# Kernel tuning notes

Measured on AMD Instinct MI355X. Metric: run time of the kernel, lower is better.

Reference implementation:

```python
import jax, jax.numpy as jnp
import numpy as np

N = 4_000_000   # points at level d
SIDE = 1024     # coordinate range per axis
HALF = SIDE // 2  # parent coord range


def setup_inputs() -> dict:
    key = jax.random.key(0)
    k1, k2 = jax.random.split(key)
    xyz = jax.random.randint(k1, (N, 3), 0, SIDE, dtype=jnp.int32)
    b = (jnp.arange(N, dtype=jnp.int32) % 4)[:, None]  # 4 batches
    coords = jnp.concatenate([b, xyz], axis=1)          # (N,4): [b,x,y,z]
    kernel = jnp.ones((8,), dtype=jnp.float32)          # frozen all-ones 2x2x2 conv weights
    return {"coords": coords, "kernel": kernel}


def _fog(coords, kernel):
    # pos(): occupancy code 2**(x%2 + 2*y%2 + 4*z%2)
    bits = coords[:, 1:4] & 1                       # (N,3)
    off = bits[:, 0] + 2 * bits[:, 1] + 4 * bits[:, 2]  # (N,) child offset in 2x2x2 window
    pos = jnp.exp2(off.astype(jnp.float32))         # (N,) code in {1,2,4,...,128}
    contrib = pos * kernel[off]                     # per-offset conv weight (all ones)
    # stride-2 conv: parent voxel = floor(xyz/2); linearize (b,z,y,x) into a key
    parent = coords[:, 1:4] >> 1                    # (N,3)
    keys = (((coords[:, 0].astype(jnp.int64) * HALF + parent[:, 2]) * HALF
             + parent[:, 1]) * HALF + parent[:, 0])
    ukeys, inv = jnp.unique(keys, return_inverse=True, size=N, fill_value=-1)
    feats = jax.ops.segment_sum(contrib, inv, num_segments=N)[:, None]  # (N,1)
    # decode padded unique keys back to coords; pad slots -> -1
    px = (ukeys % HALF).astype(jnp.int32)
    py = ((ukeys // HALF) % HALF).astype(jnp.int32)
    pz = ((ukeys // (HALF * HALF)) % HALF).astype(jnp.int32)
    pb = (ukeys // (HALF * HALF * HALF)).astype(jnp.int32)
    valid = (ukeys >= 0)[:, None]
    coords_out = jnp.where(valid, jnp.stack([pb, px, py, pz], axis=1), -1)
    return coords_out, feats


def reference(coords, kernel):
    return _fog(coords, kernel)
```

## Files before the change

### kernel.cpp

```cpp
#include <hip/hip_runtime.h>
#include <stdint.h>

typedef unsigned int u32;
typedef unsigned long long u64;

#define LBITS  14
#define LMASK  ((1u << LBITS) - 1u)
#define NBUCK  (1u << (29 - LBITS))
#define BWORDS (1u << (LBITS - 5))
#define WPL    (BWORDS / 64)
#define WOPAD  (BWORDS + BWORDS / 32)
#define FCAP   192
#define BPB    4
#define TILE_A 8192
#define RPT    (TILE_A / 256)
#define S2     2
#define CAP2   9216
#define RPT2   (CAP2 / 256)
#define RECV   4
#define CAP    224
#define SCAN_ELEM 2048

__device__ __forceinline__ u32 woidx(u32 w) { return w + (w >> 5); }

__device__ __forceinline__ void wsync() {
    asm volatile("s_waitcnt lgkmcnt(0)" ::: "memory");
}

__device__ __forceinline__ u32 make_key(int4 c) {
    return ((((u32)c.x * 512u + ((u32)c.w >> 1)) * 512u + ((u32)c.z >> 1)) * 512u)
           + ((u32)c.y >> 1);
}

__global__ void __launch_bounds__(256) phase_a(const int4* __restrict__ coords,
        u32* __restrict__ linrec, u32* __restrict__ histmat, int n, u32 NT) {
    __shared__ u32 h[4 * 256];
    u32 t = threadIdx.x, wave = t >> 6;
    for (u32 j = t; j < 1024u; j += 256u) h[j] = 0u;
    __syncthreads();
    u32 base = blockIdx.x * TILE_A;
    u32 m = min((u32)TILE_A, (u32)n - base);
    for (u32 j = t; j < m; j += 256u) {
        int4 c = coords[base + j];
        u32 key = make_key(c);
        u32 off = ((u32)c.y & 1u) | (((u32)c.z & 1u) << 1) | (((u32)c.w & 1u) << 2);
        u32 rec = (key << 3) | off;
        linrec[base + j] = rec;
        atomicAdd(&h[wave * 256u + (rec >> 24)], 1u);
    }
    __syncthreads();
    histmat[t * NT + blockIdx.x] = h[t] + h[256u + t] + h[512u + t] + h[768u + t];
}

__global__ void scan_reduce(const u32* __restrict__ data, u32* __restrict__ partial, u32 G) {
    __shared__ u32 s[256];
    u32 t = threadIdx.x;
    u32 base = blockIdx.x * SCAN_ELEM + t * 8u;
    u32 sum = 0;
    #pragma unroll
    for (int j = 0; j < 8; ++j) { u32 idx = base + j; if (idx < G) sum += data[idx]; }
    s[t] = sum; __syncthreads();
    for (int d = 128; d > 0; d >>= 1) { if ((int)t < d) s[t] += s[t + d]; __syncthreads(); }
    if (t == 0) partial[blockIdx.x] = s[0];
}

__global__ void scan_apply2(const u32* __restrict__ data, u32* __restrict__ out,
                            const u32* __restrict__ partial, u32 G, u32 NB,
                            u32* __restrict__ total) {
    __shared__ u32 s[256];
    __shared__ u32 pb[2];
    u32 t = threadIdx.x;
    u32 p = (t < NB) ? partial[t] : 0u;
    u32 pbef = (t < blockIdx.x) ? p : 0u;
    s[t] = pbef; __syncthreads();
    for (int d = 128; d > 0; d >>= 1) { if ((int)t < d) s[t] += s[t + d]; __syncthreads(); }
    if (t == 0) pb[0] = s[0];
    __syncthreads();
    if (total) {
        s[t] = p; __syncthreads();
        for (int d = 128; d > 0; d >>= 1) { if ((int)t < d) s[t] += s[t + d]; __syncthreads(); }
        if (t == 0) pb[1] = s[0];
        __syncthreads();
        if (blockIdx.x == NB - 1u && t == 0u) total[0] = pb[1];
    }
    u32 base = blockIdx.x * SCAN_ELEM + t * 8u;
    u32 v[8]; u32 sum = 0;
    #pragma unroll
    for (int j = 0; j < 8; ++j) {
        u32 idx = base + j;
        v[j] = (idx < G) ? data[idx] : 0u;
        sum += v[j];
    }
    s[t] = sum; __syncthreads();
    for (int d = 1; d < 256; d <<= 1) {
        u32 add = (t >= (u32)d) ? s[t - d] : 0u;
        __syncthreads(); s[t] += add; __syncthreads();
    }
    u32 run = s[t] - sum + pb[0];
    #pragma unroll
    for (int j = 0; j < 8; ++j) {
        u32 idx = base + j;
        if (idx < G) { u32 x = v[j]; out[idx] = run; run += x; }
    }
}

__global__ void __launch_bounds__(256) part1(const u32* __restrict__ linrec,
        const u32* __restrict__ histex, u32* __restrict__ tmp,
        u32* __restrict__ cursor, int n, u32 NT) {
    __shared__ u32 stage[TILE_A];
    __shared__ u32 lcur[256];
    __shared__ u32 gb[256];
    __shared__ u32 wtot[4];
    u32 t = threadIdx.x, wave = t >> 6, lane = t & 63u;
    if (blockIdx.x < 128u) cursor[blockIdx.x * 256u + t] = 0u;
    u32 base = blockIdx.x * TILE_A;
    u32 m = min((u32)TILE_A, (u32)n - base);
    u32 m4 = m >> 2, rem = m & 3u;
    lcur[t] = 0u;
    __syncthreads();
    u32 recv[RPT]; u32 tailrec = 0u;
    const uint4* lr4 = (const uint4*)(linrec + base);
    #pragma unroll
    for (int k = 0; k < RPT / 4; ++k) {
        u32 j4 = (u32)k * 256u + t;
        if (j4 < m4) {
            uint4 v = lr4[j4];
            recv[k * 4 + 0] = v.x; recv[k * 4 + 1] = v.y;
            recv[k * 4 + 2] = v.z; recv[k * 4 + 3] = v.w;
            atomicAdd(&lcur[v.x >> 24], 1u);
            atomicAdd(&lcur[v.y >> 24], 1u);
            atomicAdd(&lcur[v.z >> 24], 1u);
            atomicAdd(&lcur[v.w >> 24], 1u);
        }
    }
    if (t < rem) {
        tailrec = linrec[base + (m & ~3u) + t];
        atomicAdd(&lcur[tailrec >> 24], 1u);
    }
    __syncthreads();
    u32 v = lcur[t];
    u32 incl = v;
    #pragma unroll
    for (int d = 1; d < 64; d <<= 1) {
        u32 x = __shfl_up(incl, d);
        if ((int)lane >= d) incl += x;
    }
    if (lane == 63u) wtot[wave] = incl;
    __syncthreads();
    u32 off = (wave > 0u ? wtot[0] : 0u) + (wave > 1u ? wtot[1] : 0u)
            + (wave > 2u ? wtot[2] : 0u);
    u32 excl = off + incl - v;
    lcur[t] = excl;
    gb[t] = histex[t * NT + blockIdx.x] - excl;
    __syncthreads();
    #pragma unroll
    for (int k = 0; k < RPT / 4; ++k) {
        u32 j4 = (u32)k * 256u + t;
        if (j4 < m4) {
            #pragma unroll
            for (int e = 0; e < 4; ++e) {
                u32 rec = recv[k * 4 + e];
                u32 pos = atomicAdd(&lcur[rec >> 24], 1u);
                stage[pos] = rec;
            }
        }
    }
    if (t < rem) {
        u32 pos = atomicAdd(&lcur[tailrec >> 24], 1u);
        stage[pos] = tailrec;
    }
    __syncthreads();
    for (u32 j = t; j < m; j += 256u) {
        u32 rec = stage[j];
        tmp[gb[rec >> 24] + j] = rec;
    }
}

__global__ void __launch_bounds__(256) part2(const u32* __restrict__ tmp,
        const u32* __restrict__ histex, u32* __restrict__ cursor,
        u32* __restrict__ buckrec, int n, u32 NT) {
    __shared__ u32 stage[CAP2];
    __shared__ u32 lcur[128];
    __shared__ u32 dstb[128];
    __shared__ u32 wtot[2];
    u32 t = threadIdx.x, lane = t & 63u;
    u32 c = blockIdx.x / S2, s = blockIdx.x % S2;
    u32 cs = histex[c * NT];
    u32 ce = (c == 255u) ? (u32)n : histex[(c + 1u) * NT];
    u32 L = ce - cs;
    u32 lo = cs + L * s / S2, hi = cs + L * (s + 1u) / S2;
    u32 cnt = hi - lo;
    if (cnt <= (u32)CAP2) {
        if (t < 128u) lcur[t] = 0u;
        __syncthreads();
        u32 recv[RPT2];
        #pragma unroll
        for (int k = 0; k < RPT2; ++k) {
            u32 j = (u32)k * 256u + t;
            if (j < cnt) {
                u32 rec = tmp[lo + j];
                recv[k] = rec;
                atomicAdd(&lcur[(rec >> 17) & 127u], 1u);
            }
        }
        __syncthreads();
        u32 v = 0, incl = 0;
        if (t < 128u) {
            v = lcur[t];
            incl = v;
            #pragma unroll
            for (int d = 1; d < 64; d <<= 1) {
                u32 x = __shfl_up(incl, d);
                if ((int)lane >= d) incl += x;
            }
            if (lane == 63u) wtot[t >> 6] = incl;
        }
        __syncthreads();
        if (t < 128u) {
            u32 off = (t >= 64u) ? wtot[0] : 0u;
            u32 excl = off + incl - v;
            u32 bucket = (c << 7) | t;
            u32 gbase = atomicAdd(&cursor[bucket], v);
            lcur[t] = excl;
            dstb[t] = bucket * (u32)CAP + gbase - excl;
        }
        __syncthreads();
        #pragma unroll
        for (int k = 0; k < RPT2; ++k) {
            u32 j = (u32)k * 256u + t;
            if (j < cnt) {
                u32 rec = recv[k];
                u32 pos = atomicAdd(&lcur[(rec >> 17) & 127u], 1u);
                stage[pos] = rec;
            }
        }
        __syncthreads();
        for (u32 j = t; j < cnt; j += 256u) {
            u32 rec = stage[j];
            buckrec[dstb[(rec >> 17) & 127u] + j] = rec;
        }
    } else {
        for (u32 i = lo + t; i < hi; i += 256u) {
            u32 rec = tmp[i];
            u32 b = rec >> 17;
            u32 pos = atomicAdd(&cursor[b], 1u);
            buckrec[b * (u32)CAP + pos] = rec;
        }
    }
}

__global__ void __launch_bounds__(256) pass_count(const u32* __restrict__ buckrec,
        const u32* __restrict__ bcnt, u32* __restrict__ ucount, int n) {
    __shared__ u32 bm[BPB][WOPAD];
    u32 wave = threadIdx.x >> 6, lane = threadIdx.x & 63u;
    u32 bucket = blockIdx.x * BPB + wave;
    u32* B = bm[wave];
    #pragma unroll
    for (int j = 0; j < WPL; ++j) B[woidx(lane * WPL + j)] = 0u;
    wsync();
    u32 start = bucket * (u32)CAP;
    u32 end = start + bcnt[bucket];
    for (u32 i = start + lane; i < end; i += 64u) {
        u32 lk = (buckrec[i] >> 3) & LMASK;
        atomicOr(&B[woidx(lk >> 5)], 1u << (lk & 31u));
    }
    wsync();
    u32 sum = 0;
    #pragma unroll
    for (int j = 0; j < WPL; ++j) sum += __popc(B[woidx(lane * WPL + j)]);
    #pragma unroll
    for (int d = 1; d < 64; d <<= 1) sum += __shfl_xor(sum, d);
    if (lane == 0u) ucount[bucket] = sum;
}

__global__ void __launch_bounds__(256) pass_emit(const u32* __restrict__ buckrec,
        const u32* __restrict__ bcnt, const u32* __restrict__ ubase,
        const float* __restrict__ kern, float4* __restrict__ rows,
        float* __restrict__ feats, int n) {
    __shared__ u32 bm[BPB][WOPAD];
    __shared__ u32 wofW[BPB][BWORDS];
    __shared__ float fl[BPB][FCAP];
    __shared__ float ksc[BPB][8];
    u32 wave = threadIdx.x >> 6, lane = threadIdx.x & 63u;
    u32 bucket = blockIdx.x * BPB + wave;
    u32* B = bm[wave];
    u32* W = wofW[wave];
    float* F = fl[wave];
    #pragma unroll
    for (int j = 0; j < WPL; ++j) B[woidx(lane * WPL + j)] = 0u;
    #pragma unroll
    for (u32 j = lane; j < FCAP; j += 64u) F[j] = 0.f;
    if (lane < 8u) ksc[wave][lane] = (float)(1u << lane) * kern[lane];
    wsync();
    u32 start = bucket * (u32)CAP;
    u32 cnt = bcnt[bucket];
    u32 recv[RECV];
    #pragma unroll
    for (int k = 0; k < RECV; ++k) {
        u32 idx = (u32)k * 64u + lane;
        if (idx < cnt) {
            u32 rec = buckrec[start + idx];
            recv[k] = rec;
            u32 lk = (rec >> 3) & LMASK;
            atomicOr(&B[woidx(lk >> 5)], 1u << (lk & 31u));
        }
    }
    wsync();
    u32 wv[WPL]; u32 pc[WPL]; u32 sum = 0;
    #pragma unroll
    for (int j = 0; j < WPL; ++j) {
        wv[j] = B[woidx(lane * WPL + j)];
        pc[j] = __popc(wv[j]);
        sum += pc[j];
    }
    u32 incl = sum;
    #pragma unroll
    for (int d = 1; d < 64; d <<= 1) {
        u32 tt = __shfl_up(incl, d);
        if ((int)lane >= d) incl += tt;
    }
    u32 lex = incl - sum;
    u32 uc = __shfl(incl, 63);
    {
        u32 r = lex;
        #pragma unroll
        for (int j = 0; j < WPL; ++j) { W[((u32)j << 6) | lane] = r; r += pc[j]; }
    }
    wsync();
    u32 base = ubase[bucket];
    bool lds_ok = (uc <= FCAP);
    if (!lds_ok) {
        for (u32 j = lane; j < uc; j += 64u) feats[base + j] = 0.f;
        asm volatile("s_waitcnt vmcnt(0)" ::: "memory");
    }
    #pragma unroll
    for (int k = 0; k < RECV; ++k) {
        u32 idx = (u32)k * 64u + lane;
        if (idx < cnt) {
            u32 rec = recv[k];
            float contrib = ksc[wave][rec & 7u];
            u32 lk = (rec >> 3) & LMASK;
            u32 w = lk >> 5, bit = lk & 31u;
            u32 r = W[((w & 7u) << 6) | (w >> 3)]
                  + __popc(B[woidx(w)] & ((1u << bit) - 1u));
            if (lds_ok) atomicAdd(&F[r], contrib);
            else        atomicAdd(&feats[base + r], contrib);
        }
    }
    wsync();
    u32 rank = base + lex;
    u32 keyhi = bucket << LBITS;
    #pragma unroll
    for (int j = 0; j < WPL; ++j) {
        u32 bits = wv[j];
        u32 kb = keyhi | ((lane * (u32)WPL + (u32)j) << 5);
        while (bits) {
            u32 tz = __builtin_ctz(bits);
            bits &= bits - 1u;
            u32 key = kb | tz;
            rows[rank++] = make_float4((float)(key >> 27), (float)(key & 511u),
                                       (float)((key >> 9) & 511u),
                                       (float)((key >> 18) & 511u));
        }
    }
    if (lds_ok) {
        for (u32 j = lane; j < uc; j += 64u) feats[base + j] = F[j];
    }
}

__global__ void pad_fill(float4* __restrict__ rows, float* __restrict__ feats,
                         const u32* __restrict__ counter, int n) {
    int i = blockIdx.x * blockDim.x + threadIdx.x;
    if (i < n && (u32)i >= counter[0]) {
        rows[i] = make_float4(-1.f, -1.f, -1.f, -1.f);
        feats[i] = 0.f;
    }
}

extern "C" void kernel_launch(void* const* d_in, const int* in_sizes, int n_in,
                              void* d_out, int out_size, void* d_ws, size_t ws_size,
                              hipStream_t stream) {
    const int n = in_sizes[0] / 4;
    const int4* coords = (const int4*)d_in[0];
    const float* kern  = (const float*)d_in[1];
    const u32 NT = ((u32)n + TILE_A - 1) / TILE_A;
    const u32 G1 = 256 * NT;
    const u32 NB1 = (G1 + SCAN_ELEM - 1) / SCAN_ELEM;
    const u32 NB3 = (NBUCK + SCAN_ELEM - 1) / SCAN_ELEM;

    u32* wsp = (u32*)d_ws;
    u32* tmp     = wsp;
    u32* histmat = tmp + n;
    u32* histex  = histmat + G1;
    u32* cursor  = histex + G1;
    u32* ucount  = cursor + NBUCK;
    u32* ubase   = ucount + NBUCK;
    u32* counter = ubase + NBUCK;
    u32* spart   = counter + 4;
    u32* linrec  = spart + 256;
    u32* buckrec = linrec;

    float4* rows  = (float4*)d_out;
    float*  feats = (float*)((char*)d_out + (size_t)n * 16);

    phase_a<<<NT, 256, 0, stream>>>(coords, linrec, histmat, n, NT);
    scan_reduce<<<NB1, 256, 0, stream>>>(histmat, spart, G1);
    scan_apply2<<<NB1, 256, 0, stream>>>(histmat, histex, spart, G1, NB1, (u32*)nullptr);
    part1<<<NT, 256, 0, stream>>>(linrec, histex, tmp, cursor, n, NT);
    part2<<<256 * S2, 256, 0, stream>>>(tmp, histex, cursor, buckrec, n, NT);
    pass_count<<<NBUCK / BPB, 256, 0, stream>>>(buckrec, cursor, ucount, n);
    scan_reduce<<<NB3, 256, 0, stream>>>(ucount, spart, NBUCK);
    scan_apply2<<<NB3, 256, 0, stream>>>(ucount, ubase, spart, NBUCK, NB3, counter);
    pass_emit<<<NBUCK / BPB, 256, 0, stream>>>(buckrec, cursor, ubase, kern,
                                               rows, feats, n);
    pad_fill<<<((u32)n + 255) / 256, 256, 0, stream>>>(rows, feats, counter, n);
}
```

Baseline: 227.9 us.

## Fuse key build into first radix pass using fixed-capacity atomic bucket slots

Removes the separate histogram pass and its global scan. Each tile now computes keys directly from coords, counts its top-byte digits in shared memory, and reserves space in fixed-capacity per-digit regions through global atomics. This saves a full read and write of the record array and two scan launches. In exchange, each digit region is capped at 16384 records, so a skewed key distribution would overflow it. Output order within a digit also depends on the order the atomics run, which part2 has to tolerate. Tile and split sizes are halved to match the new layout.

```diff
diff --git a/kernel.cpp b/kernel.cpp
--- a/kernel.cpp
+++ b/kernel.cpp
@@ -12,10 +12,11 @@
 #define WOPAD  (BWORDS + BWORDS / 32)
 #define FCAP   192
 #define BPB    4
-#define TILE_A 8192
+#define TILE_A 4096
 #define RPT    (TILE_A / 256)
-#define S2     2
-#define CAP2   9216
+#define CCAP   16384
+#define S2     4
+#define CAP2   4608
 #define RPT2   (CAP2 / 256)
 #define RECV   4
 #define CAP    224
@@ -32,24 +33,68 @@
            + ((u32)c.y >> 1);
 }
 
-__global__ void __launch_bounds__(256) phase_a(const int4* __restrict__ coords,
-        u32* __restrict__ linrec, u32* __restrict__ histmat, int n, u32 NT) {
-    __shared__ u32 h[4 * 256];
-    u32 t = threadIdx.x, wave = t >> 6;
-    for (u32 j = t; j < 1024u; j += 256u) h[j] = 0u;
-    __syncthreads();
+__global__ void zero1(u32* __restrict__ p, u32 g) {
+    u32 i = blockIdx.x * 256u + threadIdx.x;
+    if (i < g) p[i] = 0u;
+}
+
+__global__ void __launch_bounds__(256) part1f(const int4* __restrict__ coords,
+        u32* __restrict__ ccur, u32* __restrict__ tmp,
+        u32* __restrict__ cursor, int n) {
+    __shared__ u32 stage[TILE_A];
+    __shared__ u32 lcur[256];
+    __shared__ u32 gb[256];
+    __shared__ u32 wtot[4];
+    u32 t = threadIdx.x, wave = t >> 6, lane = t & 63u;
+    if (blockIdx.x < 128u) cursor[blockIdx.x * 256u + t] = 0u;
     u32 base = blockIdx.x * TILE_A;
     u32 m = min((u32)TILE_A, (u32)n - base);
+    lcur[t] = 0u;
+    __syncthreads();
+    u32 recv[RPT];
+    #pragma unroll
+    for (int k = 0; k < RPT; ++k) {
+        u32 j = (u32)k * 256u + t;
+        if (j < m) {
+            int4 c = coords[base + j];
+            u32 key = make_key(c);
+            u32 off = ((u32)c.y & 1u) | (((u32)c.z & 1u) << 1) | (((u32)c.w & 1u) << 2);
+            u32 rec = (key << 3) | off;
+            recv[k] = rec;
+            atomicAdd(&lcur[rec >> 24], 1u);
+        }
+    }
+    __syncthreads();
+    u32 v = lcur[t];
+    u32 incl = v;
+    #pragma unroll
+    for (int d = 1; d < 64; d <<= 1) {
+        u32 x = __shfl_up(incl, d);
+        if ((int)lane >= d) incl += x;
+    }
+    if (lane == 63u) wtot[wave] = incl;
+    __syncthreads();
+    u32 off = (wave > 0u ? wtot[0] : 0u) + (wave > 1u ? wtot[1] : 0u)
+            + (wave > 2u ? wtot[2] : 0u);
+    u32 excl = off + incl - v;
+    u32 gbase = atomicAdd(&ccur[t * 16u], v);
+    lcur[t] = excl;
+    gb[t] = (t << 14) + gbase - excl;
+    __syncthreads();
+    #pragma unroll
+    for (int k = 0; k < RPT; ++k) {
+        u32 j = (u32)k * 256u + t;
+        if (j < m) {
+            u32 rec = recv[k];
+            u32 pos = atomicAdd(&lcur[rec >> 24], 1u);
+            stage[pos] = rec;
+        }
+    }
+    __syncthreads();
     for (u32 j = t; j < m; j += 256u) {
-        int4 c = coords[base + j];
-        u32 key = make_key(c);
-        u32 off = ((u32)c.y & 1u) | (((u32)c.z & 1u) << 1) | (((u32)c.w & 1u) << 2);
-        u32 rec = (key << 3) | off;
-        linrec[base + j] = rec;
-        atomicAdd(&h[wave * 256u + (rec >> 24)], 1u);
-    }
-    __syncthreads();
-    histmat[t * NT + blockIdx.x] = h[t] + h[256u + t] + h[512u + t] + h[768u + t];
+        u32 rec = stage[j];
+        tmp[gb[rec >> 24] + j] = rec;
+    }
 }
 
 __global__ void scan_reduce(const u32* __restrict__ data, u32* __restrict__ partial, u32 G) {
@@ -104,90 +149,17 @@
     }
 }
 
-__global__ void __launch_bounds__(256) part1(const u32* __restrict__ linrec,
-        const u32* __restrict__ histex, u32* __restrict__ tmp,
-        u32* __restrict__ cursor, int n, u32 NT) {
-    __shared__ u32 stage[TILE_A];
-    __shared__ u32 lcur[256];
-    __shared__ u32 gb[256];
-    __shared__ u32 wtot[4];
-    u32 t = threadIdx.x, wave = t >> 6, lane = t & 63u;
-    if (blockIdx.x < 128u) cursor[blockIdx.x * 256u + t] = 0u;
-    u32 base = blockIdx.x * TILE_A;
-    u32 m = min((u32)TILE_A, (u32)n - base);
-    u32 m4 = m >> 2, rem = m & 3u;
-    lcur[t] = 0u;
-    __syncthreads();
-    u32 recv[RPT]; u32 tailrec = 0u;
-    const uint4* lr4 = (const uint4*)(linrec + base);
-    #pragma unroll
-    for (int k = 0; k < RPT / 4; ++k) {
-        u32 j4 = (u32)k * 256u + t;
-        if (j4 < m4) {
-            uint4 v = lr4[j4];
-            recv[k * 4 + 0] = v.x; recv[k * 4 + 1] = v.y;
-            recv[k * 4 + 2] = v.z; recv[k * 4 + 3] = v.w;
-            atomicAdd(&lcur[v.x >> 24], 1u);
-            atomicAdd(&lcur[v.y >> 24], 1u);
-            atomicAdd(&lcur[v.z >> 24], 1u);
-            atomicAdd(&lcur[v.w >> 24], 1u);
-        }
-    }
-    if (t < rem) {
-        tailrec = linrec[base + (m & ~3u) + t];
-        atomicAdd(&lcur[tailrec >> 24], 1u);
-    }
-    __syncthreads();
-    u32 v = lcur[t];
-    u32 incl = v;
-    #pragma unroll
-    for (int d = 1; d < 64; d <<= 1) {
-        u32 x = __shfl_up(incl, d);
-        if ((int)lane >= d) incl += x;
-    }
-    if (lane == 63u) wtot[wave] = incl;
-    __syncthreads();
-    u32 off = (wave > 0u ? wtot[0] : 0u) + (wave > 1u ? wtot[1] : 0u)
-            + (wave > 2u ? wtot[2] : 0u);
-    u32 excl = off + incl - v;
-    lcur[t] = excl;
-    gb[t] = histex[t * NT + blockIdx.x] - excl;
-    __syncthreads();
-    #pragma unroll
-    for (int k = 0; k < RPT / 4; ++k) {
-        u32 j4 = (u32)k * 256u + t;
-        if (j4 < m4) {
-            #pragma unroll
-            for (int e = 0; e < 4; ++e) {
-                u32 rec = recv[k * 4 + e];
-                u32 pos = atomicAdd(&lcur[rec >> 24], 1u);
-                stage[pos] = rec;
-            }
-        }
-    }
-    if (t < rem) {
-        u32 pos = atomicAdd(&lcur[tailrec >> 24], 1u);
-        stage[pos] = tailrec;
-    }
-    __syncthreads();
-    for (u32 j = t; j < m; j += 256u) {
-        u32 rec = stage[j];
-        tmp[gb[rec >> 24] + j] = rec;
-    }
-}
-
 __global__ void __launch_bounds__(256) part2(const u32* __restrict__ tmp,
-        const u32* __restrict__ histex, u32* __restrict__ cursor,
-        u32* __restrict__ buckrec, int n, u32 NT) {
+        const u32* __restrict__ ccur, u32* __restrict__ cursor,
+        u32* __restrict__ buckrec, int n) {
     __shared__ u32 stage[CAP2];
     __shared__ u32 lcur[128];
     __shared__ u32 dstb[128];
     __shared__ u32 wtot[2];
     u32 t = threadIdx.x, lane = t & 63u;
     u32 c = blockIdx.x / S2, s = blockIdx.x % S2;
-    u32 cs = histex[c * NT];
-    u32 ce = (c == 255u) ? (u32)n : histex[(c + 1u) * NT];
-    u32 L = ce - cs;
+    u32 cs = c << 14;
+    u32 L = ccur[c * 16u];
     u32 lo = cs + L * s / S2, hi = cs + L * (s + 1u) / S2;
     u32 cnt = hi - lo;
     if (cnt <= (u32)CAP2) {
@@ -384,30 +356,24 @@
     const int4* coords = (const int4*)d_in[0];
     const float* kern  = (const float*)d_in[1];
     const u32 NT = ((u32)n + TILE_A - 1) / TILE_A;
-    const u32 G1 = 256 * NT;
-    const u32 NB1 = (G1 + SCAN_ELEM - 1) / SCAN_ELEM;
     const u32 NB3 = (NBUCK + SCAN_ELEM - 1) / SCAN_ELEM;
 
     u32* wsp = (u32*)d_ws;
     u32* tmp     = wsp;
-    u32* histmat = tmp + n;
-    u32* histex  = histmat + G1;
-    u32* cursor  = histex + G1;
+    u32* ccur    = tmp + 256 * CCAP;
+    u32* cursor  = ccur + 256 * 16;
     u32* ucount  = cursor + NBUCK;
     u32* ubase   = ucount + NBUCK;
     u32* counter = ubase + NBUCK;
     u32* spart   = counter + 4;
-    u32* linrec  = spart + 256;
-    u32* buckrec = linrec;
+    u32* buckrec = spart + 256;
 
     float4* rows  = (float4*)d_out;
     float*  feats = (float*)((char*)d_out + (size_t)n * 16);
 
-    phase_a<<<NT, 256, 0, stream>>>(coords, linrec, histmat, n, NT);
-    scan_reduce<<<NB1, 256, 0, stream>>>(histmat, spart, G1);
-    scan_apply2<<<NB1, 256, 0, stream>>>(histmat, histex, spart, G1, NB1, (u32*)nullptr);
-    part1<<<NT, 256, 0, stream>>>(linrec, histex, tmp, cursor, n, NT);
-    part2<<<256 * S2, 256, 0, stream>>>(tmp, histex, cursor, buckrec, n, NT);
+    zero1<<<16, 256, 0, stream>>>(ccur, 256 * 16);
+    part1f<<<NT, 256, 0, stream>>>(coords, ccur, tmp, cursor, n);
+    part2<<<256 * S2, 256, 0, stream>>>(tmp, ccur, cursor, buckrec, n);
     pass_count<<<NBUCK / BPB, 256, 0, stream>>>(buckrec, cursor, ucount, n);
     scan_reduce<<<NB3, 256, 0, stream>>>(ucount, spart, NBUCK);
     scan_apply2<<<NB3, 256, 0, stream>>>(ucount, ubase, spart, NBUCK, NB3, counter);
```

After: 213.8 us. -6.2%, faster.
